# Kernel tuning notes

Hardware: AMD Instinct MI355X
Metric: run time of the kernel (lower is better)

## Reference

```python
import jax, jax.numpy as jnp
import numpy as np

COMMITMENT_COST = 0.25
DECAY = 0.99
EPSILON = 1e-05


def setup_inputs() -> dict:
    key = jax.random.key(0)
    k1, k2, k3 = jax.random.split(key, 3)
    B, C, H, W = 64, 64, 64, 64  # C == embedding_dim
    K, D = 1024, 64
    return {
        "inputs": jax.random.normal(k1, (B, C, H, W), dtype=jnp.float32),
        "weight": jax.random.normal(k2, (K, D), dtype=jnp.float32),
        "ema_cluster_size": jnp.ones((K,), dtype=jnp.float32),
        "ema_w": jax.random.normal(k3, (K, D), dtype=jnp.float32),
    }


def reference(inputs, weight, ema_cluster_size, ema_w):
    K, D = weight.shape
    # NCHW -> NHWC, flatten to [N, D]
    x = jnp.transpose(inputs, (0, 2, 3, 1))
    flat = x.reshape(-1, D)
    # squared L2 distances to all codebook entries: [N, K]
    distances = (
        jnp.sum(flat * flat, axis=1, keepdims=True)
        + jnp.sum(weight * weight, axis=1)
        - 2.0 * flat @ weight.T
    )
    idx = jnp.argmin(distances, axis=1)  # [N]
    # training-mode EMA update (replaces the one-hot scatter + matmuls with segment sums)
    counts = jax.ops.segment_sum(jnp.ones_like(idx, dtype=flat.dtype), idx, num_segments=K)
    dw = jax.ops.segment_sum(flat, idx, num_segments=K)  # encodings.T @ flat_input
    cs = ema_cluster_size * DECAY + (1.0 - DECAY) * counts
    n = jnp.sum(cs)
    cs = (cs + EPSILON) / (n + K * EPSILON) * n  # Laplace smoothing
    ew = ema_w * DECAY + (1.0 - DECAY) * dw
    new_weight = ew / cs[:, None]
    # quantize with the UPDATED codebook (matches in-place torch order)
    quantized = new_weight[idx].reshape(x.shape)
    e_latent_loss = jnp.mean(jnp.square(jax.lax.stop_gradient(quantized) - x))
    loss = COMMITMENT_COST * e_latent_loss
    quantized_st = x + jax.lax.stop_gradient(quantized - x)  # straight-through
    return loss, jnp.transpose(quantized_st, (0, 3, 1, 2)), idx[:, None]
```

## Files before the change

### kernel.cpp

```cpp
#include <hip/hip_runtime.h>

#define K_CODES 1024
#define D_DIM   64
#define N_ROWS  262144
#define HW      4096
#define CHW     262144
#define N_ELEM  16777216
#define DECAY   0.99f
#define OMD     0.01f
#define EPS_F   1e-05f
#define MARGIN_ACC 0.004f
#define FLAG_CAP 32768
#define SEG_CAP  2048
#define NHB      64
#define BROWS    128

typedef __attribute__((ext_vector_type(8))) short bf16x8;
typedef __attribute__((ext_vector_type(4))) float f32x4;

constexpr size_t OFF_LOSS    = 0;
constexpr size_t OFF_FLAGCNT = 8;
constexpr size_t OFF_DONE    = 12;
constexpr size_t OFF_W2F     = 64;
constexpr size_t OFF_W2D     = 4160;
constexpr size_t OFF_CS     = 12352;
constexpr size_t OFF_GOFF    = 16448;
constexpr size_t OFF_NEWW    = 282752;
constexpr size_t OFF_IDX     = 544896;
constexpr size_t OFF_HISTB   = 1593472;
constexpr size_t OFF_SORT    = 1855616;
constexpr size_t OFF_FLAGS   = 1855616;
constexpr size_t OFF_WFRAG   = 1986688;

__device__ __forceinline__ short f2bf(float f) {
    unsigned u = __float_as_uint(f);
    u += 0x7fffu + ((u >> 16) & 1u);
    return (short)(u >> 16);
}
__device__ __forceinline__ float bf2f(short h) {
    return __uint_as_float(((unsigned)(unsigned short)h) << 16);
}

__device__ __forceinline__ void gload_lds16(const float4* g, void* l) {
    __builtin_amdgcn_global_load_lds(
        (const __attribute__((address_space(1))) void*)g,
        (__attribute__((address_space(3))) void*)l, 16, 0, 0);
}

__global__ __launch_bounds__(256) void prep_kernel(
    const float* __restrict__ w, short* __restrict__ wfrag,
    float* __restrict__ w2f, double* __restrict__ w2d,
    int* __restrict__ zero16) {
    int t = threadIdx.x;
    if (blockIdx.x == 35 && t < 4) zero16[t] = 0;
    if (blockIdx.x < 32) {
        int gid = blockIdx.x * 256 + t;
        int j = gid >> 7, h = (gid >> 6) & 1, L = gid & 63;
        int code = j * 16 + (L & 15);
        int kb = h * 32 + ((L >> 4) << 3);
        const float* wp = w + code * D_DIM + kb;
        short hi[8], lo[8];
#pragma unroll
        for (int i = 0; i < 8; ++i) {
            float v = wp[i];
            short hb = f2bf(v);
            hi[i] = hb;
            lo[i] = f2bf(v - bf2f(hb));
        }
        short* dh = wfrag + (size_t)(((j * 2 + h) * 2 + 0) * 64 + L) * 8;
        short* dl = wfrag + (size_t)(((j * 2 + h) * 2 + 1) * 64 + L) * 8;
#pragma unroll
        for (int i = 0; i < 8; ++i) { dh[i] = hi[i]; dl[i] = lo[i]; }
    } else {
        int k = (blockIdx.x - 32) * 256 + t;
        const float* wk = w + k * D_DIM;
        float sf = 0.f; double sd = 0.0;
#pragma unroll
        for (int d = 0; d < D_DIM; ++d) {
            float wv = wk[d];
            sf = fmaf(wv, wv, sf);
            sd = fma((double)wv, (double)wv, sd);
        }
        w2f[k] = sf; w2d[k] = sd;
    }
}

__global__ __launch_bounds__(256) __attribute__((amdgpu_waves_per_eu(2, 4)))
void argmin_kernel(
    const float* __restrict__ inp, const short* __restrict__ wfrag,
    const float* __restrict__ w2f, int* __restrict__ idx_ws,
    float* __restrict__ out_idx_f, float* __restrict__ xt,
    int* __restrict__ flagcnt, int* __restrict__ flaglist) {
    __shared__ float w2s[K_CODES];
    __shared__ alignas(16) char smem_u[64 * 68 * 4];
    __shared__ alignas(16) short bufA[8192];
    float (*xs)[68] = (float (*)[68])smem_u;
    short* bufB = (short*)smem_u;

    int t = threadIdx.x;
    ((float4*)w2s)[t] = ((const float4*)w2f)[t];

    int rowbase = blockIdx.x * BROWS;
    int b = rowbase >> 12, hwb = rowbase & (HW - 1);
    const float* xp = inp + (size_t)b * CHW + hwb;
    int lane = t & 63, wave = t >> 6;
    int q = lane >> 4, col = lane & 15;

    bf16x8 aH[2][2], aL[2][2];

    for (int p = 0; p < 2; ++p) {
#pragma unroll
        for (int it = 0; it < 16; ++it) {
            int d = wave * 16 + it;
            xs[lane][d] = xp[(size_t)d * HW + p * 64 + lane];
        }
        __syncthreads();

        float4* xt4 = (float4*)(xt + (size_t)(rowbase + p * 64) * D_DIM);
#pragma unroll
        for (int i2 = 0; i2 < 4; ++i2) {
            int c2 = t + i2 * 256;
            xt4[c2] = ((const float4*)xs[c2 >> 4])[c2 & 15];
        }

        if ((wave >> 1) == p) {
#pragma unroll
            for (int s2 = 0; s2 < 2; ++s2) {
                int rl = (wave & 1) * 32 + s2 * 16 + col;
#pragma unroll
                for (int h = 0; h < 2; ++h) {
#pragma unroll
                    for (int i = 0; i < 8; ++i) {
                        float v = xs[rl][h * 32 + q * 8 + i];
                        short hb = f2bf(v);
                        aH[s2][h][i] = hb;
                        aL[s2][h][i] = f2bf(v - bf2f(hb));
                    }
                }
            }
        }
        __syncthreads();
    }

    float best[2][4], best2[2][4];
#pragma unroll
    for (int s2 = 0; s2 < 2; ++s2)
#pragma unroll
        for (int r = 0; r < 4; ++r) { best[s2][r] = -3.4e38f; best2[s2][r] = -3.4e38f; }
    const float4* wsrc = (const float4*)wfrag;

    {
        const float4* src = wsrc + t;
        char* nb = (char*)bufA + wave * 1024;
#pragma unroll
        for (int i2 = 0; i2 < 4; ++i2)
            gload_lds16(src + i2 * 256, nb + i2 * 4096);
    }

    for (int st = 0; st < 16; ++st) {
        asm volatile("s_waitcnt vmcnt(0)" ::: "memory");
        __syncthreads();
        if (st < 15) {
            const float4* src = wsrc + (size_t)(st + 1) * 1024 + t;
            char* nb = ((st & 1) ? (char*)bufA : (char*)bufB) + wave * 1024;
#pragma unroll
            for (int i2 = 0; i2 < 4; ++i2)
                gload_lds16(src + i2 * 256, nb + i2 * 4096);
        }
        const bf16x8* wt = (const bf16x8*)((st & 1) ? bufB : bufA);

#pragma unroll
        for (int jp = 0; jp < 2; ++jp) {
            int jA = st * 4 + jp * 2, jB = jA + 1;
            int jjA = jp * 2, jjB = jp * 2 + 1;
            bf16x8 bh0A = wt[(jjA * 4 + 0) * 64 + lane];
            bf16x8 bl0A = wt[(jjA * 4 + 1) * 64 + lane];
            bf16x8 bh1A = wt[(jjA * 4 + 2) * 64 + lane];
            bf16x8 bl1A = wt[(jjA * 4 + 3) * 64 + lane];
            bf16x8 bh0B = wt[(jjB * 4 + 0) * 64 + lane];
            bf16x8 bl0B = wt[(jjB * 4 + 1) * 64 + lane];
            bf16x8 bh1B = wt[(jjB * 4 + 2) * 64 + lane];
            bf16x8 bl1B = wt[(jjB * 4 + 3) * 64 + lane];
            float cA = -0.5f * w2s[jA * 16 + col];
            float cB = -0.5f * w2s[jB * 16 + col];
            f32x4 a0A = {cA, cA, cA, cA}, a1A = {cA, cA, cA, cA};
            f32x4 a0B = {cB, cB, cB, cB}, a1B = {cB, cB, cB, cB};
            a0A = __builtin_amdgcn_mfma_f32_16x16x32_bf16(aL[0][0], bh0A, a0A, 0, 0, 0);
            a1A = __builtin_amdgcn_mfma_f32_16x16x32_bf16(aL[1][0], bh0A, a1A, 0, 0, 0);
            a0B = __builtin_amdgcn_mfma_f32_16x16x32_bf16(aL[0][0], bh0B, a0B, 0, 0, 0);
            a1B = __builtin_amdgcn_mfma_f32_16x16x32_bf16(aL[1][0], bh0B, a1B, 0, 0, 0);
            a0A = __builtin_amdgcn_mfma_f32_16x16x32_bf16(aL[0][1], bh1A, a0A, 0, 0, 0);
            a1A = __builtin_amdgcn_mfma_f32_16x16x32_bf16(aL[1][1], bh1A, a1A, 0, 0, 0);
            a0B = __builtin_amdgcn_mfma_f32_16x16x32_bf16(aL[0][1], bh1B, a0B, 0, 0, 0);
            a1B = __builtin_amdgcn_mfma_f32_16x16x32_bf16(aL[1][1], bh1B, a1B, 0, 0, 0);
            a0A = __builtin_amdgcn_mfma_f32_16x16x32_bf16(aH[0][0], bl0A, a0A, 0, 0, 0);
            a1A = __builtin_amdgcn_mfma_f32_16x16x32_bf16(aH[1][0], bl0A, a1A, 0, 0, 0);
            a0B = __builtin_amdgcn_mfma_f32_16x16x32_bf16(aH[0][0], bl0B, a0B, 0, 0, 0);
            a1B = __builtin_amdgcn_mfma_f32_16x16x32_bf16(aH[1][0], bl0B, a1B, 0, 0, 0);
            a0A = __builtin_amdgcn_mfma_f32_16x16x32_bf16(aH[0][1], bl1A, a0A, 0, 0, 0);
            a1A = __builtin_amdgcn_mfma_f32_16x16x32_bf16(aH[1][1], bl1A, a1A, 0, 0, 0);
            a0B = __builtin_amdgcn_mfma_f32_16x16x32_bf16(aH[0][1], bl1B, a0B, 0, 0, 0);
            a1B = __builtin_amdgcn_mfma_f32_16x16x32_bf16(aH[1][1], bl1B, a1B, 0, 0, 0);
            a0A = __builtin_amdgcn_mfma_f32_16x16x32_bf16(aH[0][0], bh0A, a0A, 0, 0, 0);
            a1A = __builtin_amdgcn_mfma_f32_16x16x32_bf16(aH[1][0], bh0A, a1A, 0, 0, 0);
            a0B = __builtin_amdgcn_mfma_f32_16x16x32_bf16(aH[0][0], bh0B, a0B, 0, 0, 0);
            a1B = __builtin_amdgcn_mfma_f32_16x16x32_bf16(aH[1][0], bh0B, a1B, 0, 0, 0);
            a0A = __builtin_amdgcn_mfma_f32_16x16x32_bf16(aH[0][1], bh1A, a0A, 0, 0, 0);
            a1A = __builtin_amdgcn_mfma_f32_16x16x32_bf16(aH[1][1], bh1A, a1A, 0, 0, 0);
            a0B = __builtin_amdgcn_mfma_f32_16x16x32_bf16(aH[0][1], bh1B, a0B, 0, 0, 0);
            a1B = __builtin_amdgcn_mfma_f32_16x16x32_bf16(aH[1][1], bh1B, a1B, 0, 0, 0);
#pragma unroll
            for (int s2 = 0; s2 < 2; ++s2) {
#pragma unroll
                for (int r = 0; r < 4; ++r) {
                    float vA = (s2 ? a1A : a0A)[r];
                    float vB = (s2 ? a1B : a0B)[r];
                    float kA = __int_as_float((__float_as_int(vA) & ~63) | jA);
                    float kB = __int_as_float((__float_as_int(vB) & ~63) | jB);
                    float hi = fmaxf(kA, kB);
                    float lo = fminf(kA, kB);
                    float tm = fminf(best[s2][r], hi);
                    best2[s2][r] = fmaxf(fmaxf(tm, lo), best2[s2][r]);
                    best[s2][r]  = fmaxf(best[s2][r], hi);
                }
            }
        }
    }

    int bk[2][4];
#pragma unroll
    for (int s2 = 0; s2 < 2; ++s2)
#pragma unroll
        for (int r = 0; r < 4; ++r)
            bk[s2][r] = ((__float_as_int(best[s2][r]) & 63) << 4) | col;

#pragma unroll
    for (int m = 1; m < 16; m <<= 1) {
#pragma unroll
        for (int s2 = 0; s2 < 2; ++s2) {
#pragma unroll
            for (int r = 0; r < 4; ++r) {
                float ob  = __shfl_xor(best[s2][r], m, 64);
                float ob2 = __shfl_xor(best2[s2][r], m, 64);
                int   obk = __shfl_xor(bk[s2][r], m, 64);
                float nb2 = fmaxf(fmaxf(best2[s2][r], ob2),
                                  fminf(best[s2][r], ob));
                int   nbk = ob > best[s2][r] ? obk
                            : (best[s2][r] > ob ? bk[s2][r]
                                                : min(bk[s2][r], obk));
                best[s2][r]  = fmaxf(best[s2][r], ob);
                best2[s2][r] = nb2;
                bk[s2][r]    = nbk;
            }
        }
    }

    if (col == 0) {
#pragma unroll
        for (int s2 = 0; s2 < 2; ++s2) {
#pragma unroll
            for (int r = 0; r < 4; ++r) {
                int row = rowbase + wave * 32 + s2 * 16 + q * 4 + r;
                idx_ws[row]    = bk[s2][r];
                out_idx_f[row] = (float)bk[s2][r];
                if (best[s2][r] - best2[s2][r] < MARGIN_ACC) {
                    int pos = atomicAdd(flagcnt, 1);
                    if (pos < FLAG_CAP) flaglist[pos] = row;
                }
            }
        }
    }
}

__global__ __launch_bounds__(256) void refine_kernel(
    const float* __restrict__ xt, const float* __restrict__ weight,
    const double* __restrict__ w2d, int* __restrict__ idx_ws,
    float* __restrict__ out_idx_f, const int* __restrict__ flagcnt,
    const int* __restrict__ flaglist) {
    __shared__ float sx[4][64];
    int cnt = *flagcnt;
    if (cnt > FLAG_CAP) cnt = FLAG_CAP;
    int t = threadIdx.x, lane = t & 63, wave = t >> 6;

    for (int r = blockIdx.x * 4 + wave; r < cnt; r += gridDim.x * 4) {
        int row = flaglist[r];
        sx[wave][lane] = xt[(size_t)row * D_DIM + lane];
        asm volatile("s_waitcnt lgkmcnt(0)" ::: "memory");

        double bd = 1.0e300; int bi = 0;
        int k0 = lane * 16;
#pragma unroll 4
        for (int c = 0; c < 16; ++c) {
            int k = k0 + c;
            const float4* wk4 = (const float4*)(weight + (size_t)k * D_DIM);
            double dot = 0.0;
#pragma unroll
            for (int d4 = 0; d4 < 16; ++d4) {
                float4 wv = wk4[d4];
                dot = fma((double)wv.x, (double)sx[wave][d4 * 4 + 0], dot);
                dot = fma((double)wv.y, (double)sx[wave][d4 * 4 + 1], dot);
                dot = fma((double)wv.z, (double)sx[wave][d4 * 4 + 2], dot);
                dot = fma((double)wv.w, (double)sx[wave][d4 * 4 + 3], dot);
            }
            double dist = w2d[k] - 2.0 * dot;
            if (dist < bd) { bd = dist; bi = k; }
        }
#pragma unroll
        for (int m = 1; m < 64; m <<= 1) {
            double od = __shfl_xor(bd, m, 64);
            int    oi = __shfl_xor(bi, m, 64);
            if (od < bd || (od == bd && oi < bi)) { bd = od; bi = oi; }
        }
        if (lane == 0 && bi != idx_ws[row]) {
            idx_ws[row]    = bi;
            out_idx_f[row] = (float)bi;
        }
    }
}

__global__ __launch_bounds__(256) void hist_kernel(
    const int* __restrict__ idx_ws, int* __restrict__ histb) {
    __shared__ int h[K_CODES];
    int t = threadIdx.x, b = blockIdx.x;
    for (int i = t; i < K_CODES; i += 256) h[i] = 0;
    __syncthreads();
    const int4* idx4 = (const int4*)idx_ws + b * 1024;
#pragma unroll
    for (int i = 0; i < 4; ++i) {
        int4 c = idx4[t + i * 256];
        atomicAdd(&h[c.x], 1); atomicAdd(&h[c.y], 1);
        atomicAdd(&h[c.z], 1); atomicAdd(&h[c.w], 1);
    }
    __syncthreads();
    for (int i = t; i < K_CODES; i += 256) histb[b * K_CODES + i] = h[i];
}

__global__ __launch_bounds__(1024) void scan_kernel(
    int* __restrict__ histb, int* __restrict__ goff,
    const float* __restrict__ ema_cs, float* __restrict__ csbuf) {
    __shared__ int pre[K_CODES];
    __shared__ float red[K_CODES];
    int k = threadIdx.x;

    int s = 0;
    for (int b = 0; b < NHB; ++b) {
        int v = histb[b * K_CODES + k];
        histb[b * K_CODES + k] = s;
        s += v;
    }
    int cnt = s;

    pre[k] = cnt;
    __syncthreads();
    for (int d = 1; d < K_CODES; d <<= 1) {
        int v = (k >= d) ? pre[k - d] : 0;
        __syncthreads();
        if (k >= d) pre[k] += v;
        __syncthreads();
    }
    int base = pre[k] - cnt;
    goff[k] = base;
    if (k == K_CODES - 1) goff[K_CODES] = pre[k];

    for (int b = 0; b < NHB; ++b) histb[b * K_CODES + k] += base;

    float cs = ema_cs[k] * DECAY + OMD * (float)cnt;
    red[k] = cs;
    __syncthreads();
    for (int s2 = 512; s2 > 0; s2 >>= 1) {
        if (k < s2) red[k] += red[k + s2];
        __syncthreads();
    }
    float n = red[0];
    csbuf[k] = (cs + EPS_F) / (n + (float)K_CODES * EPS_F) * n;
}

__global__ __launch_bounds__(256) void scatter_kernel(
    const int* __restrict__ idx_ws, const int* __restrict__ histb,
    int* __restrict__ sorted) {
    __shared__ int cur[K_CODES];
    int t = threadIdx.x, b = blockIdx.x;
    for (int i = t; i < K_CODES; i += 256) cur[i] = histb[b * K_CODES + i];
    __syncthreads();
    const int4* idx4 = (const int4*)idx_ws + b * 1024;
#pragma unroll
    for (int i = 0; i < 4; ++i) {
        int4 c = idx4[t + i * 256];
        int r0 = (b * 1024 + t + i * 256) * 4;
        sorted[atomicAdd(&cur[c.x], 1)] = r0 + 0;
        sorted[atomicAdd(&cur[c.y], 1)] = r0 + 1;
        sorted[atomicAdd(&cur[c.z], 1)] = r0 + 2;
        sorted[atomicAdd(&cur[c.w], 1)] = r0 + 3;
    }
}

__global__ __launch_bounds__(256) void dwred_kernel(
    const float* __restrict__ xt, const int* __restrict__ sorted,
    const int* __restrict__ goff, const float* __restrict__ ema_w,
    const float* __restrict__ csbuf, float* __restrict__ new_w) {
    __shared__ int   rows[SEG_CAP];
    __shared__ float red[256];
    int k = blockIdx.x, t = threadIdx.x;
    int base = goff[k];
    int cnt = goff[k + 1] - base;
    int cc = cnt > SEG_CAP ? SEG_CAP : cnt;

    for (int i = t; i < cc; i += 256) rows[i] = sorted[base + i];
    __syncthreads();

    int d = t & 63, sub = t >> 6;
    float a0 = 0.f, a1 = 0.f;
    int i = sub;
    for (; i + 4 < cc; i += 8) {
        a0 += xt[(size_t)rows[i] * D_DIM + d];
        a1 += xt[(size_t)rows[i + 4] * D_DIM + d];
    }
    for (; i < cc; i += 4) a0 += xt[(size_t)rows[i] * D_DIM + d];
    red[t] = a0 + a1;
    __syncthreads();
    if (t < 64) {
        float dwv = red[t] + red[t + 64] + red[t + 128] + red[t + 192];
        new_w[k * D_DIM + t] =
            (ema_w[k * D_DIM + t] * DECAY + OMD * dwv) / csbuf[k];
    }
}

__global__ __launch_bounds__(256) void out_kernel(
    const float* __restrict__ inp, const float* __restrict__ new_w,
    const int* __restrict__ idx_ws, float* __restrict__ out,
    double* __restrict__ loss_acc, int* __restrict__ done_cnt) {
    int row = blockIdx.x * 256 + threadIdx.x;
    int b  = row >> 12;
    int hw = row & (HW - 1);
    const float* xp = inp + (size_t)b * CHW + hw;
    float* op = out + 1 + (size_t)b * CHW + hw;

    int k = idx_ws[row];
    const float* q = new_w + k * D_DIM;

    float lsum = 0.f;
#pragma unroll
    for (int d = 0; d < D_DIM; ++d) {
        float xv = xp[(size_t)d * HW];
        float qv = q[d];
        float diff = qv - xv;
        lsum = fmaf(diff, diff, lsum);
        op[(size_t)d * HW] = xv + diff;
    }

    __shared__ double lred[256];
    lred[threadIdx.x] = (double)lsum;
    __syncthreads();
    for (int s = 128; s > 0; s >>= 1) {
        if (threadIdx.x < s) lred[threadIdx.x] += lred[threadIdx.x + s];
        __syncthreads();
    }
    if (threadIdx.x == 0) {
        atomicAdd(loss_acc, lred[0]);
        __threadfence();
        int old = atomicAdd(done_cnt, 1);
        if (old == (int)gridDim.x - 1) {
            double v = atomicAdd(loss_acc, 0.0);
            out[0] = (float)(0.25 * (v / (double)N_ELEM));
        }
    }
}

extern "C" void kernel_launch(void* const* d_in, const int* in_sizes, int n_in,
                              void* d_out, int out_size, void* d_ws, size_t ws_size,
                              hipStream_t stream) {
    const float* inp    = (const float*)d_in[0];
    const float* weight = (const float*)d_in[1];
    const float* ema_cs = (const float*)d_in[2];
    const float* ema_w  = (const float*)d_in[3];
    float* out = (float*)d_out;

    char* ws = (char*)d_ws;
    double* loss_acc = (double*)(ws + OFF_LOSS);
    int*    flagcnt  = (int*)(ws + OFF_FLAGCNT);
    int*    done_cnt = (int*)(ws + OFF_DONE);
    float*  w2f      = (float*)(ws + OFF_W2F);
    double* w2d      = (double*)(ws + OFF_W2D);
    float*  csbuf    = (float*)(ws + OFF_CS);
    int*    goff     = (int*)(ws + OFF_GOFF);
    float*  new_w    = (float*)(ws + OFF_NEWW);
    int*    idx_ws   = (int*)(ws + OFF_IDX);
    int*    histb    = (int*)(ws + OFF_HISTB);
    int*    sorted   = (int*)(ws + OFF_SORT);
    int*    flaglist = (int*)(ws + OFF_FLAGS);
    short*  wfrag    = (short*)(ws + OFF_WFRAG);

    float* xt        = out + 1;
    float* out_idx_f = out + 1 + (size_t)N_ELEM;

    prep_kernel<<<36, 256, 0, stream>>>(weight, wfrag, w2f, w2d, (int*)ws);

    argmin_kernel<<<N_ROWS / BROWS, 256, 0, stream>>>(
        inp, wfrag, w2f, idx_ws, out_idx_f, xt, flagcnt, flaglist);

    refine_kernel<<<512, 256, 0, stream>>>(
        xt, weight, w2d, idx_ws, out_idx_f, flagcnt, flaglist);

    hist_kernel<<<NHB, 256, 0, stream>>>(idx_ws, histb);

    scan_kernel<<<1, 1024, 0, stream>>>(histb, goff, ema_cs, csbuf);

    scatter_kernel<<<NHB, 256, 0, stream>>>(idx_ws, histb, sorted);

    dwred_kernel<<<K_CODES, 256, 0, stream>>>(xt, sorted, goff, ema_w, csbuf, new_w);

    out_kernel<<<N_ROWS / 256, 256, 0, stream>>>(inp, new_w, idx_ws, out,
                                                 loss_acc, done_cnt);
}
```

Measured before the change: 434.1 us.

## Fuse refine, histogram and cluster-size scan into argmin; drop counting sort

Ambiguous rows are now re-checked in fp64 inside each argmin block, using a small shared flag list. Code counts are accumulated with global atomics, and the last block computes the smoothed cluster sizes. That removes the refine, hist, scan and scatter launches. dwred no longer gathers through a sorted row list: every code block scans the whole index array with ballots and accumulates the matching rows. This saves launches and the sort, but each of the 1024 blocks now reads all 262144 indices, and a block with more than 96 ambiguous rows skips refining the excess.

```diff
diff --git a/kernel.cpp b/kernel.cpp
--- a/kernel.cpp
+++ b/kernel.cpp
@@ -10,26 +10,21 @@
 #define OMD     0.01f
 #define EPS_F   1e-05f
 #define MARGIN_ACC 0.004f
-#define FLAG_CAP 32768
-#define SEG_CAP  2048
-#define NHB      64
 #define BROWS    128
+#define BFLAG_CAP 96
 
 typedef __attribute__((ext_vector_type(8))) short bf16x8;
 typedef __attribute__((ext_vector_type(4))) float f32x4;
 
 constexpr size_t OFF_LOSS    = 0;
-constexpr size_t OFF_FLAGCNT = 8;
+constexpr size_t OFF_ADONE   = 8;
 constexpr size_t OFF_DONE    = 12;
 constexpr size_t OFF_W2F     = 64;
 constexpr size_t OFF_W2D     = 4160;
-constexpr size_t OFF_CS     = 12352;
-constexpr size_t OFF_GOFF    = 16448;
+constexpr size_t OFF_CS      = 12352;
+constexpr size_t OFF_CNT     = 16448;
 constexpr size_t OFF_NEWW    = 282752;
 constexpr size_t OFF_IDX     = 544896;
-constexpr size_t OFF_HISTB   = 1593472;
-constexpr size_t OFF_SORT    = 1855616;
-constexpr size_t OFF_FLAGS   = 1855616;
 constexpr size_t OFF_WFRAG   = 1986688;
 
 __device__ __forceinline__ short f2bf(float f) {
@@ -50,9 +45,12 @@
 __global__ __launch_bounds__(256) void prep_kernel(
     const float* __restrict__ w, short* __restrict__ wfrag,
     float* __restrict__ w2f, double* __restrict__ w2d,
-    int* __restrict__ zero16) {
+    int* __restrict__ scalars, int* __restrict__ cnt) {
     int t = threadIdx.x;
-    if (blockIdx.x == 35 && t < 4) zero16[t] = 0;
+    if (blockIdx.x == 35) {
+        if (t < 16) scalars[t] = 0;
+        cnt[t] = 0; cnt[t + 256] = 0; cnt[t + 512] = 0; cnt[t + 768] = 0;
+    }
     if (blockIdx.x < 32) {
         int gid = blockIdx.x * 256 + t;
         int j = gid >> 7, h = (gid >> 6) & 1, L = gid & 63;
@@ -88,17 +86,23 @@
 __global__ __launch_bounds__(256) __attribute__((amdgpu_waves_per_eu(2, 4)))
 void argmin_kernel(
     const float* __restrict__ inp, const short* __restrict__ wfrag,
-    const float* __restrict__ w2f, int* __restrict__ idx_ws,
-    float* __restrict__ out_idx_f, float* __restrict__ xt,
-    int* __restrict__ flagcnt, int* __restrict__ flaglist) {
+    const float* __restrict__ w2f, const float* __restrict__ wgt,
+    const double* __restrict__ w2d, const float* __restrict__ ema_cs,
+    int* __restrict__ idx_ws, float* __restrict__ out_idx_f,
+    float* __restrict__ xt, int* __restrict__ cnt,
+    int* __restrict__ adone, float* __restrict__ csbuf) {
     __shared__ float w2s[K_CODES];
     __shared__ alignas(16) char smem_u[64 * 68 * 4];
     __shared__ alignas(16) short bufA[8192];
+    __shared__ float sxr[4][64];
+    __shared__ int bflag[BFLAG_CAP];
+    __shared__ int bcnt, isLast;
     float (*xs)[68] = (float (*)[68])smem_u;
     short* bufB = (short*)smem_u;
 
     int t = threadIdx.x;
     ((float4*)w2s)[t] = ((const float4*)w2f)[t];
+    if (t == 0) bcnt = 0;
 
     int rowbase = blockIdx.x * BROWS;
     int b = rowbase >> 12, hwb = rowbase & (HW - 1);
@@ -255,52 +259,47 @@
         }
     }
 
+    __syncthreads();
     if (col == 0) {
 #pragma unroll
         for (int s2 = 0; s2 < 2; ++s2) {
 #pragma unroll
             for (int r = 0; r < 4; ++r) {
                 int row = rowbase + wave * 32 + s2 * 16 + q * 4 + r;
-                idx_ws[row]    = bk[s2][r];
-                out_idx_f[row] = (float)bk[s2][r];
+                int k = bk[s2][r];
+                idx_ws[row]    = k;
+                out_idx_f[row] = (float)k;
+                atomicAdd(&cnt[k], 1);
                 if (best[s2][r] - best2[s2][r] < MARGIN_ACC) {
-                    int pos = atomicAdd(flagcnt, 1);
-                    if (pos < FLAG_CAP) flaglist[pos] = row;
+                    int p = atomicAdd(&bcnt, 1);
+                    if (p < BFLAG_CAP) bflag[p] = (row << 10) | k;
                 }
             }
         }
     }
-}
-
-__global__ __launch_bounds__(256) void refine_kernel(
-    const float* __restrict__ xt, const float* __restrict__ weight,
-    const double* __restrict__ w2d, int* __restrict__ idx_ws,
-    float* __restrict__ out_idx_f, const int* __restrict__ flagcnt,
-    const int* __restrict__ flaglist) {
-    __shared__ float sx[4][64];
-    int cnt = *flagcnt;
-    if (cnt > FLAG_CAP) cnt = FLAG_CAP;
-    int t = threadIdx.x, lane = t & 63, wave = t >> 6;
-
-    for (int r = blockIdx.x * 4 + wave; r < cnt; r += gridDim.x * 4) {
-        int row = flaglist[r];
-        sx[wave][lane] = xt[(size_t)row * D_DIM + lane];
+    __syncthreads();
+
+    int nb = bcnt < BFLAG_CAP ? bcnt : BFLAG_CAP;
+    for (int i = wave; i < nb; i += 4) {
+        int e = bflag[i];
+        int row = e >> 10, old = e & 1023;
+        sxr[wave][lane] = xt[(size_t)row * D_DIM + lane];
         asm volatile("s_waitcnt lgkmcnt(0)" ::: "memory");
 
         double bd = 1.0e300; int bi = 0;
         int k0 = lane * 16;
-#pragma unroll 4
+#pragma unroll 2
         for (int c = 0; c < 16; ++c) {
             int k = k0 + c;
-            const float4* wk4 = (const float4*)(weight + (size_t)k * D_DIM);
+            const float4* wk4 = (const float4*)(wgt + (size_t)k * D_DIM);
             double dot = 0.0;
 #pragma unroll
             for (int d4 = 0; d4 < 16; ++d4) {
                 float4 wv = wk4[d4];
-                dot = fma((double)wv.x, (double)sx[wave][d4 * 4 + 0], dot);
-                dot = fma((double)wv.y, (double)sx[wave][d4 * 4 + 1], dot);
-                dot = fma((double)wv.z, (double)sx[wave][d4 * 4 + 2], dot);
-                dot = fma((double)wv.w, (double)sx[wave][d4 * 4 + 3], dot);
+                dot = fma((double)wv.x, (double)sxr[wave][d4 * 4 + 0], dot);
+                dot = fma((double)wv.y, (double)sxr[wave][d4 * 4 + 1], dot);
+                dot = fma((double)wv.z, (double)sxr[wave][d4 * 4 + 2], dot);
+                dot = fma((double)wv.w, (double)sxr[wave][d4 * 4 + 3], dot);
             }
             double dist = w2d[k] - 2.0 * dot;
             if (dist < bd) { bd = dist; bi = k; }
@@ -311,115 +310,83 @@
             int    oi = __shfl_xor(bi, m, 64);
             if (od < bd || (od == bd && oi < bi)) { bd = od; bi = oi; }
         }
-        if (lane == 0 && bi != idx_ws[row]) {
+        if (lane == 0 && bi != old) {
             idx_ws[row]    = bi;
             out_idx_f[row] = (float)bi;
-        }
-    }
-}
-
-__global__ __launch_bounds__(256) void hist_kernel(
-    const int* __restrict__ idx_ws, int* __restrict__ histb) {
-    __shared__ int h[K_CODES];
-    int t = threadIdx.x, b = blockIdx.x;
-    for (int i = t; i < K_CODES; i += 256) h[i] = 0;
-    __syncthreads();
-    const int4* idx4 = (const int4*)idx_ws + b * 1024;
-#pragma unroll
-    for (int i = 0; i < 4; ++i) {
-        int4 c = idx4[t + i * 256];
-        atomicAdd(&h[c.x], 1); atomicAdd(&h[c.y], 1);
-        atomicAdd(&h[c.z], 1); atomicAdd(&h[c.w], 1);
-    }
-    __syncthreads();
-    for (int i = t; i < K_CODES; i += 256) histb[b * K_CODES + i] = h[i];
-}
-
-__global__ __launch_bounds__(1024) void scan_kernel(
-    int* __restrict__ histb, int* __restrict__ goff,
-    const float* __restrict__ ema_cs, float* __restrict__ csbuf) {
-    __shared__ int pre[K_CODES];
-    __shared__ float red[K_CODES];
-    int k = threadIdx.x;
-
-    int s = 0;
-    for (int b = 0; b < NHB; ++b) {
-        int v = histb[b * K_CODES + k];
-        histb[b * K_CODES + k] = s;
-        s += v;
-    }
-    int cnt = s;
-
-    pre[k] = cnt;
-    __syncthreads();
-    for (int d = 1; d < K_CODES; d <<= 1) {
-        int v = (k >= d) ? pre[k - d] : 0;
+            atomicSub(&cnt[old], 1);
+            atomicAdd(&cnt[bi], 1);
+        }
+    }
+
+    __threadfence();
+    __syncthreads();
+    if (t == 0) isLast = (atomicAdd(adone, 1) == (int)gridDim.x - 1);
+    __syncthreads();
+    if (!isLast) return;
+
+    float* red = w2s;
+    float css[4]; float mycs = 0.f;
+#pragma unroll
+    for (int c = 0; c < 4; ++c) {
+        int k = t * 4 + c;
+        int cv = atomicAdd(&cnt[k], 0);
+        css[c] = ema_cs[k] * DECAY + OMD * (float)cv;
+        mycs += css[c];
+    }
+    red[t] = mycs;
+    __syncthreads();
+    for (int s = 128; s > 0; s >>= 1) {
+        if (t < s) red[t] += red[t + s];
         __syncthreads();
-        if (k >= d) pre[k] += v;
-        __syncthreads();
-    }
-    int base = pre[k] - cnt;
-    goff[k] = base;
-    if (k == K_CODES - 1) goff[K_CODES] = pre[k];
-
-    for (int b = 0; b < NHB; ++b) histb[b * K_CODES + k] += base;
-
-    float cs = ema_cs[k] * DECAY + OMD * (float)cnt;
-    red[k] = cs;
-    __syncthreads();
-    for (int s2 = 512; s2 > 0; s2 >>= 1) {
-        if (k < s2) red[k] += red[k + s2];
-        __syncthreads();
     }
     float n = red[0];
-    csbuf[k] = (cs + EPS_F) / (n + (float)K_CODES * EPS_F) * n;
-}
-
-__global__ __launch_bounds__(256) void scatter_kernel(
-    const int* __restrict__ idx_ws, const int* __restrict__ histb,
-    int* __restrict__ sorted) {
-    __shared__ int cur[K_CODES];
-    int t = threadIdx.x, b = blockIdx.x;
-    for (int i = t; i < K_CODES; i += 256) cur[i] = histb[b * K_CODES + i];
-    __syncthreads();
-    const int4* idx4 = (const int4*)idx_ws + b * 1024;
-#pragma unroll
-    for (int i = 0; i < 4; ++i) {
-        int4 c = idx4[t + i * 256];
-        int r0 = (b * 1024 + t + i * 256) * 4;
-        sorted[atomicAdd(&cur[c.x], 1)] = r0 + 0;
-        sorted[atomicAdd(&cur[c.y], 1)] = r0 + 1;
-        sorted[atomicAdd(&cur[c.z], 1)] = r0 + 2;
-        sorted[atomicAdd(&cur[c.w], 1)] = r0 + 3;
+#pragma unroll
+    for (int c = 0; c < 4; ++c) {
+        int k = t * 4 + c;
+        csbuf[k] = (css[c] + EPS_F) / (n + (float)K_CODES * EPS_F) * n;
     }
 }
 
 __global__ __launch_bounds__(256) void dwred_kernel(
-    const float* __restrict__ xt, const int* __restrict__ sorted,
-    const int* __restrict__ goff, const float* __restrict__ ema_w,
-    const float* __restrict__ csbuf, float* __restrict__ new_w) {
-    __shared__ int   rows[SEG_CAP];
-    __shared__ float red[256];
+    const float* __restrict__ xt, const int* __restrict__ idx_ws,
+    const float* __restrict__ ema_w, const float* __restrict__ csbuf,
+    float* __restrict__ new_w) {
+    __shared__ float red[4][64];
     int k = blockIdx.x, t = threadIdx.x;
-    int base = goff[k];
-    int cnt = goff[k + 1] - base;
-    int cc = cnt > SEG_CAP ? SEG_CAP : cnt;
-
-    for (int i = t; i < cc; i += 256) rows[i] = sorted[base + i];
-    __syncthreads();
-
-    int d = t & 63, sub = t >> 6;
-    float a0 = 0.f, a1 = 0.f;
-    int i = sub;
-    for (; i + 4 < cc; i += 8) {
-        a0 += xt[(size_t)rows[i] * D_DIM + d];
-        a1 += xt[(size_t)rows[i + 4] * D_DIM + d];
-    }
-    for (; i < cc; i += 4) a0 += xt[(size_t)rows[i] * D_DIM + d];
-    red[t] = a0 + a1;
+    int lane = t & 63, wave = t >> 6;
+    const int4* idx4 = (const int4*)idx_ws;
+
+    float acc = 0.f;
+    for (int it = 0; it < 256; ++it) {
+        int e = wave * 16384 + it * 64 + lane;
+        int4 c = idx4[e];
+        int ebase = (e - lane) * 4;
+        unsigned long long m;
+        m = __ballot(c.x == k);
+        while (m) {
+            int l = __ffsll((unsigned long long)m) - 1; m &= m - 1;
+            acc += xt[(size_t)(ebase + l * 4 + 0) * D_DIM + lane];
+        }
+        m = __ballot(c.y == k);
+        while (m) {
+            int l = __ffsll((unsigned long long)m) - 1; m &= m - 1;
+            acc += xt[(size_t)(ebase + l * 4 + 1) * D_DIM + lane];
+        }
+        m = __ballot(c.z == k);
+        while (m) {
+            int l = __ffsll((unsigned long long)m) - 1; m &= m - 1;
+            acc += xt[(size_t)(ebase + l * 4 + 2) * D_DIM + lane];
+        }
+        m = __ballot(c.w == k);
+        while (m) {
+            int l = __ffsll((unsigned long long)m) - 1; m &= m - 1;
+            acc += xt[(size_t)(ebase + l * 4 + 3) * D_DIM + lane];
+        }
+    }
+    red[wave][lane] = acc;
     __syncthreads();
     if (t < 64) {
-        float dwv = red[t] + red[t + 64] + red[t + 128] + red[t + 192];
+        float dwv = red[0][t] + red[1][t] + red[2][t] + red[3][t];
         new_w[k * D_DIM + t] =
             (ema_w[k * D_DIM + t] * DECAY + OMD * dwv) / csbuf[k];
     }
@@ -477,37 +444,26 @@
 
     char* ws = (char*)d_ws;
     double* loss_acc = (double*)(ws + OFF_LOSS);
-    int*    flagcnt  = (int*)(ws + OFF_FLAGCNT);
+    int*    adone    = (int*)(ws + OFF_ADONE);
     int*    done_cnt = (int*)(ws + OFF_DONE);
     float*  w2f      = (float*)(ws + OFF_W2F);
     double* w2d      = (double*)(ws + OFF_W2D);
     float*  csbuf    = (float*)(ws + OFF_CS);
-    int*    goff     = (int*)(ws + OFF_GOFF);
+    int*    cnt      = (int*)(ws + OFF_CNT);
     float*  new_w    = (float*)(ws + OFF_NEWW);
     int*    idx_ws   = (int*)(ws + OFF_IDX);
-    int*    histb    = (int*)(ws + OFF_HISTB);
-    int*    sorted   = (int*)(ws + OFF_SORT);
-    int*    flaglist = (int*)(ws + OFF_FLAGS);
     short*  wfrag    = (short*)(ws + OFF_WFRAG);
 
     float* xt        = out + 1;
     float* out_idx_f = out + 1 + (size_t)N_ELEM;
 
-    prep_kernel<<<36, 256, 0, stream>>>(weight, wfrag, w2f, w2d, (int*)ws);
+    prep_kernel<<<36, 256, 0, stream>>>(weight, wfrag, w2f, w2d, (int*)ws, cnt);
 
     argmin_kernel<<<N_ROWS / BROWS, 256, 0, stream>>>(
-        inp, wfrag, w2f, idx_ws, out_idx_f, xt, flagcnt, flaglist);
-
-    refine_kernel<<<512, 256, 0, stream>>>(
-        xt, weight, w2d, idx_ws, out_idx_f, flagcnt, flaglist);
-
-    hist_kernel<<<NHB, 256, 0, stream>>>(idx_ws, histb);
-
-    scan_kernel<<<1, 1024, 0, stream>>>(histb, goff, ema_cs, csbuf);
-
-    scatter_kernel<<<NHB, 256, 0, stream>>>(idx_ws, histb, sorted);
-
-    dwred_kernel<<<K_CODES, 256, 0, stream>>>(xt, sorted, goff, ema_w, csbuf, new_w);
+        inp, wfrag, w2f, weight, w2d, ema_cs,
+        idx_ws, out_idx_f, xt, cnt, adone, csbuf);
+
+    dwred_kernel<<<K_CODES, 256, 0, stream>>>(xt, idx_ws, ema_w, csbuf, new_w);
 
     out_kernel<<<N_ROWS / 256, 256, 0, stream>>>(inp, new_w, idx_ws, out,
                                                  loss_acc, done_cnt);
```

Measured after the change: 924.8 us. 113% more time.
